# Kernel tuning notes

Measured on AMD Instinct MI355X. Metric: run time of the kernel, lower is better.

The kernel has to match this reference:

```python
import jax, jax.numpy as jnp
import numpy as np

DIM = 1024
HEADS = 16
DIM_HEAD = DIM // HEADS

def setup_inputs() -> dict:
    key = jax.random.key(0)
    k1, k2, k3 = jax.random.split(key, 3)
    x = jax.random.normal(k1, (2, 2048, DIM), dtype=jnp.float32)
    # nn.Linear(dim, 3*dim, bias=False): weight [3*dim, dim]; y = x @ W.T
    W_qkv = jax.random.normal(k2, (3 * DIM, DIM), dtype=jnp.float32) * (1.0 / np.sqrt(DIM))
    W_out = jax.random.normal(k3, (DIM, DIM), dtype=jnp.float32) * (1.0 / np.sqrt(DIM))
    return {"x": x, "W_qkv": W_qkv, "W_out": W_out}

def reference(x, W_qkv, W_out):
    b, s, _ = x.shape
    scale = DIM_HEAD ** -0.5
    qkv = x @ W_qkv.T                              # [b, s, 3*dim]
    q, k, v = jnp.split(qkv, 3, axis=-1)
    def to_heads(t):
        return t.reshape(b, s, HEADS, DIM_HEAD).transpose(0, 2, 1, 3)  # [b,h,s,d]
    q, k, v = map(to_heads, (q, k, v))
    scores = jnp.einsum('bhid,bhjd->bhij', q, k) * scale
    causal_mask = jnp.triu(jnp.ones((s, s), dtype=bool), k=1)
    scores = jnp.where(causal_mask, -jnp.inf, scores)
    attn = jax.nn.softmax(scores, axis=-1)
    out = jnp.einsum('bhij,bhjd->bhid', attn, v)
    out = out.transpose(0, 2, 1, 3).reshape(b, s, HEADS * DIM_HEAD)
    return out @ W_out.T
```

## Files before the change

### kernel.cpp

```cpp
#include <hip/hip_runtime.h>
#include <hip/hip_bf16.h>
#include <math.h>

using bf16 = __hip_bfloat16;
typedef __attribute__((ext_vector_type(8))) short bf16x8;
typedef __attribute__((ext_vector_type(4))) short bf16x4;
typedef __attribute__((ext_vector_type(4))) float f32x4;
typedef __attribute__((ext_vector_type(2))) int i32x2;

static __device__ __forceinline__ void gl_lds16(const void* g, void* l) {
  __builtin_amdgcn_global_load_lds(
      (const __attribute__((address_space(1))) unsigned int*)g,
      (__attribute__((address_space(3))) unsigned int*)l, 16, 0, 0);
}

#define MFMA16 __builtin_amdgcn_mfma_f32_16x16x32_bf16
#define MFMA16K16 __builtin_amdgcn_mfma_f32_16x16x16bf16_1k

static __device__ __forceinline__ short f2bf(float f) {
  return (short)((__builtin_bit_cast(unsigned int, f) + 0x8000u) >> 16);
}

__global__ __launch_bounds__(256) void cvt_all(
    const float* __restrict__ x, const float* __restrict__ wqkv,
    const float* __restrict__ wout, bf16* __restrict__ xb,
    bf16* __restrict__ wqkvb, bf16* __restrict__ woutb) {
  const int blk = blockIdx.x;
  const float* src;
  bf16* dst;
  int base;
  if (blk < 4096) {
    src = x; dst = xb; base = blk;
  } else if (blk < 7168) {
    src = wqkv; dst = wqkvb; base = blk - 4096;
  } else {
    src = wout; dst = woutb; base = blk - 7168;
  }
  const int i = (base * 256 + threadIdx.x) * 4;
  const float4 v = *(const float4*)(src + i);
  bf16x4 o;
  o.x = f2bf(v.x);
  o.y = f2bf(v.y);
  o.z = f2bf(v.z);
  o.w = f2bf(v.w);
  *(bf16x4*)(dst + i) = o;
}

template <int K>
static __device__ __forceinline__ void gemm_bt_acc(
    const bf16* __restrict__ A, const bf16* __restrict__ B,
    int rowA0, int rowB0, bf16* As, bf16* Bs, f32x4 acc[4][4]) {
  const int t = threadIdx.x;
  const int w = t >> 6, l = t & 63;
  const int quad = l >> 4, l16 = l & 15;
  const int wm = (w >> 1) * 64, wn = (w & 1) * 64;
  const int c0 = t, c1 = t + 256;
  const bf16* a0 = A + (size_t)(rowA0 + (c0 >> 2)) * K + (c0 & 3) * 8;
  const bf16* a1 = A + (size_t)(rowA0 + (c1 >> 2)) * K + (c1 & 3) * 8;
  const bf16* b0 = B + (size_t)(rowB0 + (c0 >> 2)) * K + (c0 & 3) * 8;
  const bf16* b1 = B + (size_t)(rowB0 + (c1 >> 2)) * K + (c1 & 3) * 8;
  for (int k0 = 0; k0 < K; k0 += 32) {
    __syncthreads();
    gl_lds16(a0 + k0, As + c0 * 8);
    gl_lds16(a1 + k0, As + c1 * 8);
    gl_lds16(b0 + k0, Bs + c0 * 8);
    gl_lds16(b1 + k0, Bs + c1 * 8);
    __syncthreads();
    bf16x8 af[4], bg[4];
#pragma unroll
    for (int i = 0; i < 4; i++)
      af[i] = *(const bf16x8*)(As + (wm + i * 16 + l16) * 32 + quad * 8);
#pragma unroll
    for (int j = 0; j < 4; j++)
      bg[j] = *(const bf16x8*)(Bs + (wn + j * 16 + l16) * 32 + quad * 8);
#pragma unroll
    for (int i = 0; i < 4; i++)
#pragma unroll
      for (int j = 0; j < 4; j++)
        acc[i][j] = MFMA16(af[i], bg[j], acc[i][j], 0, 0, 0);
  }
}

__global__ __launch_bounds__(256) void qkv_gemm(
    const bf16* __restrict__ x, const bf16* __restrict__ Wqkv,
    bf16* __restrict__ Qb, bf16* __restrict__ Kb, bf16* __restrict__ Vt) {
  __shared__ bf16 As[128 * 32];
  __shared__ bf16 Bs[128 * 32];
  f32x4 acc[4][4];
#pragma unroll
  for (int i = 0; i < 4; i++)
#pragma unroll
    for (int j = 0; j < 4; j++) acc[i][j] = (f32x4){0.f, 0.f, 0.f, 0.f};
  const int bm = blockIdx.x, bn = blockIdx.y;
  gemm_bt_acc<1024>(x, Wqkv, bm * 128, bn * 128, As, Bs, acc);

  const int t = threadIdx.x, w = t >> 6, l = t & 63;
  const int quad = l >> 4, l16 = l & 15;
  const int wm = (w >> 1) * 64, wn = (w & 1) * 64;
#pragma unroll
  for (int i = 0; i < 4; i++) {
    const int m0 = bm * 128 + wm + i * 16 + quad * 4;
    const int b = m0 >> 11, s0 = m0 & 2047;
#pragma unroll
    for (int j = 0; j < 4; j++) {
      const int n = bn * 128 + wn + j * 16 + l16;
      const int which = n >> 10;
      const int nn = n & 1023;
      const int h = nn >> 6, d = nn & 63;
      const int bh = b * 16 + h;
      if (which == 2) {
        bf16x4 v4;
#pragma unroll
        for (int r = 0; r < 4; r++)
          v4[r] = (short)__builtin_bit_cast(unsigned short,
                                            __float2bfloat16(acc[i][j][r]));
        *(bf16x4*)(Vt + ((size_t)bh * 64 + d) * 2048 + s0) = v4;
      } else {
        const float sc = (which == 0) ? 0.125f : 1.0f;
        bf16* dst = (which == 0) ? Qb : Kb;
#pragma unroll
        for (int r = 0; r < 4; r++)
          dst[((size_t)bh * 2048 + s0 + r) * 64 + d] =
              __float2bfloat16(acc[i][j][r] * sc);
      }
    }
  }
}

__global__ __launch_bounds__(256) void attn_kernel(
    const bf16* __restrict__ Qb, const bf16* __restrict__ Kb,
    const bf16* __restrict__ Vt, bf16* __restrict__ attn) {
  __shared__ bf16 Qs[64 * 64];
  __shared__ bf16 Ks[128 * 64];
  __shared__ bf16 Vts[64 * 128];
  const int x = blockIdx.x;
  const int bh = x & 31;
  const int idx = x >> 5;
  const int t = threadIdx.x, w = t >> 6, l = t & 63;
  const int quad = l >> 4, l16 = l & 15;
  const bf16x4 ones = {16256, 16256, 16256, 16256};
  const int b = bh >> 4, h = bh & 15;

  for (int pass = 0; pass < 2; pass++) {
    const int qt = pass ? 31 - idx : idx;
    const int q0 = qt * 64;
    if (pass) __syncthreads();

    const bf16* Qg = Qb + ((size_t)bh * 2048 + q0) * 64;
#pragma unroll
    for (int c = t; c < 512; c += 256) {
      const int row = c >> 3, pos = c & 7;
      gl_lds16(Qg + (row * 8 + (pos ^ (row & 7))) * 8, Qs + c * 8);
    }

    f32x4 oacc[4];
    f32x4 lacc = (f32x4){0.f, 0.f, 0.f, 0.f};
#pragma unroll
    for (int md = 0; md < 4; md++) oacc[md] = (f32x4){0.f, 0.f, 0.f, 0.f};

    const int njj = (qt + 2) >> 1;
    for (int jj = 0; jj < njj; jj++) {
      const int j0 = jj * 128;
      __syncthreads();
      const bf16* Kg = Kb + ((size_t)bh * 2048 + j0) * 64;
#pragma unroll
      for (int c = t; c < 1024; c += 256) {
        const int row = c >> 3, pos = c & 7;
        gl_lds16(Kg + (row * 8 + (pos ^ (row & 7))) * 8, Ks + c * 8);
      }
      const bf16* Vg = Vt + (size_t)bh * 64 * 2048 + j0;
#pragma unroll
      for (int c = t; c < 1024; c += 256) {
        const int d = c >> 4, pos = c & 15;
        gl_lds16(Vg + (size_t)d * 2048 + ((pos ^ (d & 15)) * 8), Vts + c * 8);
      }
      __syncthreads();

      f32x4 sacc[8];
#pragma unroll
      for (int mt = 0; mt < 8; mt++) sacc[mt] = (f32x4){0.f, 0.f, 0.f, 0.f};
#pragma unroll
      for (int kk = 0; kk < 2; kk++) {
        const int qrow = w * 16 + l16;
        const int qpos = (kk * 4 + quad) ^ (qrow & 7);
        bf16x8 qf = *(const bf16x8*)(Qs + qrow * 64 + qpos * 8);
#pragma unroll
        for (int mt = 0; mt < 8; mt++) {
          const int row = mt * 16 + l16;
          const int pos = (kk * 4 + quad) ^ (row & 7);
          bf16x8 kf = *(const bf16x8*)(Ks + row * 64 + pos * 8);
          sacc[mt] = MFMA16(kf, qf, sacc[mt], 0, 0, 0);
        }
      }

      bf16x4 pfrag[8];
      if (jj == njj - 1) {
        const int qi = q0 + w * 16 + l16;
#pragma unroll
        for (int mt = 0; mt < 8; mt++) {
          unsigned rb[4];
#pragma unroll
          for (int r = 0; r < 4; r++) {
            const int sg = j0 + mt * 16 + quad * 4 + r;
            const float p = (sg <= qi) ? __expf(sacc[mt][r]) : 0.f;
            rb[r] = __builtin_bit_cast(unsigned, p) + 0x8000u;
          }
          i32x2 pk;
          pk.x = (int)__builtin_amdgcn_perm(rb[1], rb[0], 0x07060302u);
          pk.y = (int)__builtin_amdgcn_perm(rb[3], rb[2], 0x07060302u);
          pfrag[mt] = __builtin_bit_cast(bf16x4, pk);
        }
      } else {
#pragma unroll
        for (int mt = 0; mt < 8; mt++) {
          unsigned rb[4];
#pragma unroll
          for (int r = 0; r < 4; r++) {
            const float p = __expf(sacc[mt][r]);
            rb[r] = __builtin_bit_cast(unsigned, p) + 0x8000u;
          }
          i32x2 pk;
          pk.x = (int)__builtin_amdgcn_perm(rb[1], rb[0], 0x07060302u);
          pk.y = (int)__builtin_amdgcn_perm(rb[3], rb[2], 0x07060302u);
          pfrag[mt] = __builtin_bit_cast(bf16x4, pk);
        }
      }

#pragma unroll
      for (int kt = 0; kt < 8; kt++) {
        lacc = MFMA16K16(ones, pfrag[kt], lacc, 0, 0, 0);
#pragma unroll
        for (int md = 0; md < 4; md++) {
          const int d = md * 16 + l16;
          const int pos = (kt * 2 + (quad >> 1)) ^ (d & 15);
          bf16x4 va =
              *(const bf16x4*)(Vts + d * 128 + pos * 8 + (quad & 1) * 4);
          oacc[md] = MFMA16K16(va, pfrag[kt], oacc[md], 0, 0, 0);
        }
      }
    }

    const float inv = 1.0f / lacc[0];
    const int srow = q0 + w * 16 + l16;
#pragma unroll
    for (int md = 0; md < 4; md++) {
      bf16x4 o4;
#pragma unroll
      for (int r = 0; r < 4; r++) o4[r] = f2bf(oacc[md][r] * inv);
      *(bf16x4*)(attn + ((size_t)b * 2048 + srow) * 1024 + h * 64 + md * 16 +
                 quad * 4) = o4;
    }
  }
}

__global__ __launch_bounds__(256) void out_gemm(
    const bf16* __restrict__ attn, const bf16* __restrict__ Wout,
    float* __restrict__ out) {
  __shared__ bf16 As[128 * 32];
  __shared__ bf16 Bs[64 * 32];
  f32x4 acc[4][2];
#pragma unroll
  for (int i = 0; i < 4; i++)
#pragma unroll
    for (int j = 0; j < 2; j++) acc[i][j] = (f32x4){0.f, 0.f, 0.f, 0.f};
  const int bm = blockIdx.x, bn = blockIdx.y;
  const int t = threadIdx.x, w = t >> 6, l = t & 63;
  const int quad = l >> 4, l16 = l & 15;
  const int wm = (w >> 1) * 64, wn = (w & 1) * 32;
  const int c0 = t, c1 = t + 256;
  const bf16* a0 = attn + (size_t)(bm * 128 + (c0 >> 2)) * 1024 + (c0 & 3) * 8;
  const bf16* a1 = attn + (size_t)(bm * 128 + (c1 >> 2)) * 1024 + (c1 & 3) * 8;
  const bf16* b0 = Wout + (size_t)(bn * 64 + (t >> 2)) * 1024 + (t & 3) * 8;
  for (int k0 = 0; k0 < 1024; k0 += 32) {
    __syncthreads();
    gl_lds16(a0 + k0, As + c0 * 8);
    gl_lds16(a1 + k0, As + c1 * 8);
    gl_lds16(b0 + k0, Bs + t * 8);
    __syncthreads();
    bf16x8 af[4], bg[2];
#pragma unroll
    for (int i = 0; i < 4; i++)
      af[i] = *(const bf16x8*)(As + (wm + i * 16 + l16) * 32 + quad * 8);
#pragma unroll
    for (int j = 0; j < 2; j++)
      bg[j] = *(const bf16x8*)(Bs + (wn + j * 16 + l16) * 32 + quad * 8);
#pragma unroll
    for (int i = 0; i < 4; i++)
#pragma unroll
      for (int j = 0; j < 2; j++)
        acc[i][j] = MFMA16(af[i], bg[j], acc[i][j], 0, 0, 0);
  }
#pragma unroll
  for (int i = 0; i < 4; i++) {
#pragma unroll
    for (int j = 0; j < 2; j++) {
      const int n = bn * 64 + wn + j * 16 + l16;
#pragma unroll
      for (int r = 0; r < 4; r++) {
        const int m = bm * 128 + wm + i * 16 + quad * 4 + r;
        out[(size_t)m * 1024 + n] = acc[i][j][r];
      }
    }
  }
}

extern "C" void kernel_launch(void* const* d_in, const int* in_sizes, int n_in,
                              void* d_out, int out_size, void* d_ws, size_t ws_size,
                              hipStream_t stream) {
  const float* x = (const float*)d_in[0];
  const float* Wqkv = (const float*)d_in[1];
  const float* Wout = (const float*)d_in[2];
  float* out = (float*)d_out;

  char* ws = (char*)d_ws;
  const size_t MB = 1024 * 1024;
  bf16* xb = (bf16*)(ws + 0 * MB);
  bf16* at = (bf16*)(ws + 0 * MB);
  bf16* Wqkvb = (bf16*)(ws + 8 * MB);
  bf16* Woutb = (bf16*)(ws + 14 * MB);
  bf16* Qb = (bf16*)(ws + 16 * MB);
  bf16* Kb = (bf16*)(ws + 24 * MB);
  bf16* Vt = (bf16*)(ws + 32 * MB);

  cvt_all<<<8192, 256, 0, stream>>>(x, Wqkv, Wout, xb, Wqkvb, Woutb);
  qkv_gemm<<<dim3(32, 24), 256, 0, stream>>>(xb, Wqkvb, Qb, Kb, Vt);
  attn_kernel<<<512, 256, 0, stream>>>(Qb, Kb, Vt, at);
  out_gemm<<<dim3(32, 16), 256, 0, stream>>>(at, Woutb, out);
}
```

Measured before the change: 166.1 us.

## Enlarge attention query tile to 128 rows, one tile per block

Each attention block now processes a single 128-row query tile, with each wave covering 32 rows as two 16-row sub-tiles, instead of two balanced 64-row passes. Every K fragment loaded from LDS and every staged K/V chunk now feeds twice as many MFMAs, which cuts LDS reads and global K/V traffic per unit of work. The cost is higher register pressure from doubled accumulators. It also drops the paired short/long tile scheme, so per-block work now ranges from 1 to 16 key chunks, which risks load imbalance across CUs.

```diff
diff --git a/kernel.cpp b/kernel.cpp
--- a/kernel.cpp
+++ b/kernel.cpp
@@ -130,123 +130,143 @@
 __global__ __launch_bounds__(256) void attn_kernel(
     const bf16* __restrict__ Qb, const bf16* __restrict__ Kb,
     const bf16* __restrict__ Vt, bf16* __restrict__ attn) {
-  __shared__ bf16 Qs[64 * 64];
+  __shared__ bf16 Qs[128 * 64];
   __shared__ bf16 Ks[128 * 64];
   __shared__ bf16 Vts[64 * 128];
   const int x = blockIdx.x;
   const int bh = x & 31;
   const int idx = x >> 5;
+  const int qt = (idx < 8) ? idx : 23 - idx;
+  const int q0 = qt * 128;
   const int t = threadIdx.x, w = t >> 6, l = t & 63;
   const int quad = l >> 4, l16 = l & 15;
   const bf16x4 ones = {16256, 16256, 16256, 16256};
   const int b = bh >> 4, h = bh & 15;
 
-  for (int pass = 0; pass < 2; pass++) {
-    const int qt = pass ? 31 - idx : idx;
-    const int q0 = qt * 64;
-    if (pass) __syncthreads();
-
-    const bf16* Qg = Qb + ((size_t)bh * 2048 + q0) * 64;
-#pragma unroll
-    for (int c = t; c < 512; c += 256) {
+  const bf16* Qg = Qb + ((size_t)bh * 2048 + q0) * 64;
+#pragma unroll
+  for (int c = t; c < 1024; c += 256) {
+    const int row = c >> 3, pos = c & 7;
+    gl_lds16(Qg + (row * 8 + (pos ^ (row & 7))) * 8, Qs + c * 8);
+  }
+
+  f32x4 oacc[2][4];
+  f32x4 lacc[2];
+#pragma unroll
+  for (int nt = 0; nt < 2; nt++) {
+    lacc[nt] = (f32x4){0.f, 0.f, 0.f, 0.f};
+#pragma unroll
+    for (int md = 0; md < 4; md++) oacc[nt][md] = (f32x4){0.f, 0.f, 0.f, 0.f};
+  }
+
+  const int njj = qt + 1;
+  for (int jj = 0; jj < njj; jj++) {
+    const int j0 = jj * 128;
+    __syncthreads();
+    const bf16* Kg = Kb + ((size_t)bh * 2048 + j0) * 64;
+#pragma unroll
+    for (int c = t; c < 1024; c += 256) {
       const int row = c >> 3, pos = c & 7;
-      gl_lds16(Qg + (row * 8 + (pos ^ (row & 7))) * 8, Qs + c * 8);
-    }
-
-    f32x4 oacc[4];
-    f32x4 lacc = (f32x4){0.f, 0.f, 0.f, 0.f};
-#pragma unroll
-    for (int md = 0; md < 4; md++) oacc[md] = (f32x4){0.f, 0.f, 0.f, 0.f};
-
-    const int njj = (qt + 2) >> 1;
-    for (int jj = 0; jj < njj; jj++) {
-      const int j0 = jj * 128;
-      __syncthreads();
-      const bf16* Kg = Kb + ((size_t)bh * 2048 + j0) * 64;
-#pragma unroll
-      for (int c = t; c < 1024; c += 256) {
-        const int row = c >> 3, pos = c & 7;
-        gl_lds16(Kg + (row * 8 + (pos ^ (row & 7))) * 8, Ks + c * 8);
-      }
-      const bf16* Vg = Vt + (size_t)bh * 64 * 2048 + j0;
-#pragma unroll
-      for (int c = t; c < 1024; c += 256) {
-        const int d = c >> 4, pos = c & 15;
-        gl_lds16(Vg + (size_t)d * 2048 + ((pos ^ (d & 15)) * 8), Vts + c * 8);
-      }
-      __syncthreads();
-
-      f32x4 sacc[8];
-#pragma unroll
-      for (int mt = 0; mt < 8; mt++) sacc[mt] = (f32x4){0.f, 0.f, 0.f, 0.f};
-#pragma unroll
-      for (int kk = 0; kk < 2; kk++) {
-        const int qrow = w * 16 + l16;
+      gl_lds16(Kg + (row * 8 + (pos ^ (row & 7))) * 8, Ks + c * 8);
+    }
+    const bf16* Vg = Vt + (size_t)bh * 64 * 2048 + j0;
+#pragma unroll
+    for (int c = t; c < 1024; c += 256) {
+      const int d = c >> 4, pos = c & 15;
+      gl_lds16(Vg + (size_t)d * 2048 + ((pos ^ (d & 15)) * 8), Vts + c * 8);
+    }
+    __syncthreads();
+
+    f32x4 sacc[2][8];
+#pragma unroll
+    for (int nt = 0; nt < 2; nt++)
+#pragma unroll
+      for (int mt = 0; mt < 8; mt++) sacc[nt][mt] = (f32x4){0.f, 0.f, 0.f, 0.f};
+#pragma unroll
+    for (int kk = 0; kk < 2; kk++) {
+      bf16x8 qf[2];
+#pragma unroll
+      for (int nt = 0; nt < 2; nt++) {
+        const int qrow = w * 32 + nt * 16 + l16;
         const int qpos = (kk * 4 + quad) ^ (qrow & 7);
-        bf16x8 qf = *(const bf16x8*)(Qs + qrow * 64 + qpos * 8);
-#pragma unroll
-        for (int mt = 0; mt < 8; mt++) {
-          const int row = mt * 16 + l16;
-          const int pos = (kk * 4 + quad) ^ (row & 7);
-          bf16x8 kf = *(const bf16x8*)(Ks + row * 64 + pos * 8);
-          sacc[mt] = MFMA16(kf, qf, sacc[mt], 0, 0, 0);
-        }
-      }
-
-      bf16x4 pfrag[8];
-      if (jj == njj - 1) {
-        const int qi = q0 + w * 16 + l16;
+        qf[nt] = *(const bf16x8*)(Qs + qrow * 64 + qpos * 8);
+      }
+#pragma unroll
+      for (int mt = 0; mt < 8; mt++) {
+        const int row = mt * 16 + l16;
+        const int pos = (kk * 4 + quad) ^ (row & 7);
+        bf16x8 kf = *(const bf16x8*)(Ks + row * 64 + pos * 8);
+#pragma unroll
+        for (int nt = 0; nt < 2; nt++)
+          sacc[nt][mt] = MFMA16(kf, qf[nt], sacc[nt][mt], 0, 0, 0);
+      }
+    }
+
+    bf16x4 pfrag[2][8];
+    if (jj == njj - 1) {
+#pragma unroll
+      for (int nt = 0; nt < 2; nt++) {
+        const int qi = q0 + w * 32 + nt * 16 + l16;
 #pragma unroll
         for (int mt = 0; mt < 8; mt++) {
           unsigned rb[4];
 #pragma unroll
           for (int r = 0; r < 4; r++) {
             const int sg = j0 + mt * 16 + quad * 4 + r;
-            const float p = (sg <= qi) ? __expf(sacc[mt][r]) : 0.f;
+            const float p = (sg <= qi) ? __expf(sacc[nt][mt][r]) : 0.f;
             rb[r] = __builtin_bit_cast(unsigned, p) + 0x8000u;
           }
           i32x2 pk;
           pk.x = (int)__builtin_amdgcn_perm(rb[1], rb[0], 0x07060302u);
           pk.y = (int)__builtin_amdgcn_perm(rb[3], rb[2], 0x07060302u);
-          pfrag[mt] = __builtin_bit_cast(bf16x4, pk);
+          pfrag[nt][mt] = __builtin_bit_cast(bf16x4, pk);
         }
-      } else {
+      }
+    } else {
+#pragma unroll
+      for (int nt = 0; nt < 2; nt++) {
 #pragma unroll
         for (int mt = 0; mt < 8; mt++) {
           unsigned rb[4];
 #pragma unroll
           for (int r = 0; r < 4; r++) {
-            const float p = __expf(sacc[mt][r]);
+            const float p = __expf(sacc[nt][mt][r]);
             rb[r] = __builtin_bit_cast(unsigned, p) + 0x8000u;
           }
           i32x2 pk;
           pk.x = (int)__builtin_amdgcn_perm(rb[1], rb[0], 0x07060302u);
           pk.y = (int)__builtin_amdgcn_perm(rb[3], rb[2], 0x07060302u);
-          pfrag[mt] = __builtin_bit_cast(bf16x4, pk);
+          pfrag[nt][mt] = __builtin_bit_cast(bf16x4, pk);
         }
       }
-
-#pragma unroll
-      for (int kt = 0; kt < 8; kt++) {
-        lacc = MFMA16K16(ones, pfrag[kt], lacc, 0, 0, 0);
-#pragma unroll
-        for (int md = 0; md < 4; md++) {
-          const int d = md * 16 + l16;
-          const int pos = (kt * 2 + (quad >> 1)) ^ (d & 15);
-          bf16x4 va =
-              *(const bf16x4*)(Vts + d * 128 + pos * 8 + (quad & 1) * 4);
-          oacc[md] = MFMA16K16(va, pfrag[kt], oacc[md], 0, 0, 0);
-        }
-      }
-    }
-
-    const float inv = 1.0f / lacc[0];
-    const int srow = q0 + w * 16 + l16;
+    }
+
+#pragma unroll
+    for (int kt = 0; kt < 8; kt++) {
+#pragma unroll
+      for (int nt = 0; nt < 2; nt++)
+        lacc[nt] = MFMA16K16(ones, pfrag[nt][kt], lacc[nt], 0, 0, 0);
+#pragma unroll
+      for (int md = 0; md < 4; md++) {
+        const int d = md * 16 + l16;
+        const int pos = (kt * 2 + (quad >> 1)) ^ (d & 15);
+        bf16x4 va = *(const bf16x4*)(Vts + d * 128 + pos * 8 + (quad & 1) * 4);
+#pragma unroll
+        for (int nt = 0; nt < 2; nt++)
+          oacc[nt][md] = MFMA16K16(va, pfrag[nt][kt], oacc[nt][md], 0, 0, 0);
+      }
+    }
+  }
+
+#pragma unroll
+  for (int nt = 0; nt < 2; nt++) {
+    const float inv = 1.0f / lacc[nt][0];
+    const int srow = q0 + w * 32 + nt * 16 + l16;
 #pragma unroll
     for (int md = 0; md < 4; md++) {
       bf16x4 o4;
 #pragma unroll
-      for (int r = 0; r < 4; r++) o4[r] = f2bf(oacc[md][r] * inv);
+      for (int r = 0; r < 4; r++) o4[r] = f2bf(oacc[nt][md][r] * inv);
       *(bf16x4*)(attn + ((size_t)b * 2048 + srow) * 1024 + h * 64 + md * 16 +
                  quad * 4) = o4;
     }
```

Result: slower. 176.7 us (+6.4%).
